# Kernel optimization log

Hardware: AMD Instinct MI355X
Metric: run time of the kernel (lower is better)

The kernel has to match this reference:

```python
import jax, jax.numpy as jnp
import numpy as np

B, IN, C, H, E = 8192, 768, 64, 64, 16  # batch, input_dim, n_concepts, hidden_dim, embedding_dim


def setup_inputs() -> dict:
    key = jax.random.key(0)
    ks = jax.random.split(key, 10)

    def w(k, shape, fan_in):
        return jax.random.normal(k, shape, jnp.float32) / np.float32(np.sqrt(fan_in))

    inp = {"x": jax.random.normal(ks[0], (B, IN), jnp.float32)}
    i = 1
    for pre, din, dout in (("pos", IN, E), ("neg", IN, E), ("cp", 2 * E, 1)):
        inp[pre + "_W1"] = w(ks[i], (C, din, H), din)
        inp[pre + "_b1"] = jnp.zeros((C, H), jnp.float32)
        inp[pre + "_W2"] = w(ks[i + 1], (C, H, H), H)
        inp[pre + "_b2"] = jnp.zeros((C, H), jnp.float32)
        inp[pre + "_W3"] = w(ks[i + 2], (C, H, dout), H)
        inp[pre + "_b3"] = jnp.zeros((C, dout), jnp.float32)
        i += 3
    return inp


def _bank(x, W1, b1, W2, b2, W3, b3):
    # x: [B, IN]; per-concept MLP batched over C via einsum -> [B, C, E]
    h = jax.nn.relu(jnp.einsum('bi,cih->bch', x, W1) + b1)
    h = jax.nn.relu(jnp.einsum('bch,cho->bco', h, W2) + b2)
    return jnp.einsum('bch,che->bce', h, W3) + b3


def reference(x, pos_W1, pos_b1, pos_W2, pos_b2, pos_W3, pos_b3,
              neg_W1, neg_b1, neg_W2, neg_b2, neg_W3, neg_b3,
              cp_W1, cp_b1, cp_W2, cp_b2, cp_W3, cp_b3):
    pos = _bank(x, pos_W1, pos_b1, pos_W2, pos_b2, pos_W3, pos_b3)  # [B,C,E]
    neg = _bank(x, neg_W1, neg_b1, neg_W2, neg_b2, neg_W3, neg_b3)  # [B,C,E]
    # torch cat([pos, neg], dim=1) on [B,E,C], then x[:,:,i] -> per-concept [B, 2E]
    xc = jnp.concatenate([pos, neg], axis=-1)  # [B,C,2E]
    h = jax.nn.relu(jnp.einsum('bci,cih->bch', xc, cp_W1) + cp_b1)
    h = jax.nn.relu(jnp.einsum('bch,cho->bco', h, cp_W2) + cp_b2)
    concepts = (jnp.einsum('bch,cho->bco', h, cp_W3) + cp_b3)[..., 0]  # [B,C]
    w = jnp.clip(concepts * 0.5 + 0.5, 0.0, 1.0)[:, :, None]  # gate in [0,1]
    emb = pos * w + neg * (1.0 - w)  # [B,C,E]
    # torch layout is [B,E,C] then .view(B,-1): transpose before flattening
    emb_flat = jnp.transpose(emb, (0, 2, 1)).reshape(x.shape[0], E * C)
    return emb_flat, concepts
```

## Files before the change

### kernel.cpp

```cpp
#include <hip/hip_runtime.h>
#include <hip/hip_bf16.h>


#define B_   8192
#define IN_  768
#define C_   64
#define H_   64
#define E_   16
#define BM_  128

typedef __bf16 bf16x8 __attribute__((ext_vector_type(8)));
typedef float  f32x4  __attribute__((ext_vector_type(4)));

__device__ __forceinline__ f32x4 mfma16(bf16x8 a, bf16x8 b, f32x4 c) {
  return __builtin_amdgcn_mfma_f32_16x16x32_bf16(a, b, c, 0, 0, 0);
}

__device__ __forceinline__ bf16x8 cvt8(float4 a, float4 b) {
  bf16x8 r;
  r[0] = (__bf16)a.x; r[1] = (__bf16)a.y; r[2] = (__bf16)a.z; r[3] = (__bf16)a.w;
  r[4] = (__bf16)b.x; r[5] = (__bf16)b.y; r[6] = (__bf16)b.z; r[7] = (__bf16)b.w;
  return r;
}

__device__ __forceinline__ void zero_acc(f32x4 (&acc)[2][4]) {
  const f32x4 z = {0.f, 0.f, 0.f, 0.f};
#pragma unroll
  for (int mt = 0; mt < 2; ++mt)
#pragma unroll
    for (int nt = 0; nt < 4; ++nt) acc[mt][nt] = z;
}

__device__ __forceinline__ void gll16(const __bf16* g, __bf16* l) {
  __builtin_amdgcn_global_load_lds(
      (const __attribute__((address_space(1))) unsigned int*)g,
      (__attribute__((address_space(3))) unsigned int*)l, 16, 0, 0);
}

#define FENCE asm volatile("" ::: "memory")

struct __align__(16) SmemT {
  __bf16 bufA[256 * 64];
  __bf16 bufB[256 * 64];
  __bf16 xcb[BM_ * 40];
  float  conc[BM_];
};
static_assert(sizeof(SmemT) == 76288, "layout");
static_assert(sizeof(SmemT) <= 81920, "LDS: need 2 blocks/CU");

__device__ __forceinline__ void epi72(__bf16* __restrict__ hb, f32x4 (&acc)[2][4],
                                      const float* __restrict__ bias,
                                      int wave, int quad, int l16) {
#pragma unroll
  for (int nt = 0; nt < 4; ++nt) {
    const int col = nt * 16 + l16;
    const float bv = bias[col];
#pragma unroll
    for (int mt = 0; mt < 2; ++mt)
#pragma unroll
      for (int r = 0; r < 4; ++r) {
        int row = wave * 32 + mt * 16 + quad * 4 + r;
        hb[row * 72 + col] = (__bf16)fmaxf(acc[mt][nt][r] + bv, 0.f);
      }
  }
}

__device__ __forceinline__ void gemm64(const __bf16* __restrict__ hb,
                                       const __bf16* __restrict__ wt,
                                       f32x4 (&acc)[2][4], int wave, int quad, int l16) {
#pragma unroll
  for (int ks = 0; ks < 2; ++ks) {
    bf16x8 a[2], bb[4];
#pragma unroll
    for (int mt = 0; mt < 2; ++mt)
      a[mt] = *(const bf16x8*)(hb + (wave * 32 + mt * 16 + l16) * 72 + ks * 32 + quad * 8);
#pragma unroll
    for (int nt = 0; nt < 4; ++nt)
      bb[nt] = *(const bf16x8*)(wt + (nt * 16 + l16) * 72 + ks * 32 + quad * 8);
#pragma unroll
    for (int mt = 0; mt < 2; ++mt)
#pragma unroll
      for (int nt = 0; nt < 4; ++nt)
        acc[mt][nt] = mfma16(a[mt], bb[nt], acc[mt][nt]);
  }
}

__device__ __forceinline__ void stage_w64(const __bf16* __restrict__ Wt,
                                          __bf16* __restrict__ wt, int tid) {
#pragma unroll
  for (int it = 0; it < 2; ++it) {
    int q = tid + it * 256;
    int n = q >> 3, i = q & 7;
    *(uint4*)&wt[n * 72 + i * 8] = *(const uint4*)(Wt + n * 64 + i * 8);
  }
}

__device__ __forceinline__ void l3_tile(const __bf16* __restrict__ hb,
                                        const __bf16* __restrict__ wt16,
                                        __bf16* __restrict__ xcb,
                                        const float* __restrict__ b3, int xc_off,
                                        int wave, int quad, int l16) {
  f32x4 acc3[2];
  { const f32x4 z = {0.f, 0.f, 0.f, 0.f}; acc3[0] = z; acc3[1] = z; }
#pragma unroll
  for (int ks = 0; ks < 2; ++ks) {
    bf16x8 bb = *(const bf16x8*)(wt16 + l16 * 72 + ks * 32 + quad * 8);
#pragma unroll
    for (int mt = 0; mt < 2; ++mt) {
      bf16x8 a = *(const bf16x8*)(hb + (wave * 32 + mt * 16 + l16) * 72 + ks * 32 + quad * 8);
      acc3[mt] = mfma16(a, bb, acc3[mt]);
    }
  }
  const float bv = b3[l16];
#pragma unroll
  for (int mt = 0; mt < 2; ++mt)
#pragma unroll
    for (int r = 0; r < 4; ++r) {
      int row = wave * 32 + mt * 16 + quad * 4 + r;
      xcb[row * 40 + xc_off + l16] = (__bf16)(acc3[mt][r] + bv);
    }
}

__device__ __forceinline__ void l1_step(const __bf16* __restrict__ cbuf,
                                        f32x4 (&accP)[2][4], f32x4 (&accN)[2][4],
                                        int wave, int quad, int l16) {
  const int sx = l16 & 7;
#pragma unroll
  for (int ks = 0; ks < 2; ++ks) {
    const int pc = (((ks * 4 + quad) ^ sx)) * 8;
    bf16x8 a[2], bp[4], bn[4];
#pragma unroll
    for (int mt = 0; mt < 2; ++mt)
      a[mt] = *(const bf16x8*)(cbuf + (wave * 32 + mt * 16 + l16) * 64 + pc);
#pragma unroll
    for (int nt = 0; nt < 4; ++nt) {
      bp[nt] = *(const bf16x8*)(cbuf + (128 + nt * 16 + l16) * 64 + pc);
      bn[nt] = *(const bf16x8*)(cbuf + (192 + nt * 16 + l16) * 64 + pc);
    }
#pragma unroll
    for (int mt = 0; mt < 2; ++mt)
#pragma unroll
      for (int nt = 0; nt < 4; ++nt) {
        accP[mt][nt] = mfma16(a[mt], bp[nt], accP[mt][nt]);
        accN[mt][nt] = mfma16(a[mt], bn[nt], accN[mt][nt]);
      }
  }
}

__global__ __launch_bounds__(256, 2) void cb_fused_t(
    const __bf16* __restrict__ x,
    const __bf16* __restrict__ pW1t, const float* __restrict__ pb1,
    const __bf16* __restrict__ pW2t, const float* __restrict__ pb2,
    const __bf16* __restrict__ pW3t, const float* __restrict__ pb3,
    const __bf16* __restrict__ nW1t, const float* __restrict__ nb1,
    const __bf16* __restrict__ nW2t, const float* __restrict__ nb2,
    const __bf16* __restrict__ nW3t, const float* __restrict__ nb3,
    const __bf16* __restrict__ cW1t, const float* __restrict__ cb1,
    const __bf16* __restrict__ cW2t, const float* __restrict__ cb2,
    const __bf16* __restrict__ cw3,  const float* __restrict__ cb3,
    float* __restrict__ out_emb, float* __restrict__ out_con)
{
  __shared__ SmemT sm;
  const int tid  = threadIdx.x;
  const int wave = tid >> 6, lane = tid & 63;
  const int quad = lane >> 4, l16 = lane & 15;
  const int row0 = blockIdx.x * BM_;
  const int c    = blockIdx.y;
  __bf16* hb = sm.bufA;
  __bf16* wt = sm.bufB;

  const __bf16* pg   = pW1t + (size_t)c * 64 * IN_;
  const __bf16* ng   = nW1t + (size_t)c * 64 * IN_;
  const float*  pb1c = pb1 + c * 64;
  const float*  nb1c = nb1 + c * 64;
  const float*  pb2c = pb2 + c * 64;
  const float*  nb2c = nb2 + c * 64;

  f32x4 accP[2][4]; zero_acc(accP);
  f32x4 accN[2][4]; zero_acc(accN);

  const __bf16* xg = x + (size_t)row0 * IN_;
  const int lrow   = lane >> 3;
  const int lchunk = (lane & 7) ^ lrow;
  const __bf16* gsrc = (wave == 0) ? xg
                     : (wave == 1) ? xg + 64 * IN_
                     : (wave == 2) ? pg : ng;
  const __bf16* gl = gsrc + (size_t)lrow * IN_ + lchunk * 8;
  __bf16* const dA = sm.bufA + wave * 64 * 64;
  __bf16* const dB = sm.bufB + wave * 64 * 64;

#pragma unroll
  for (int j = 0; j < 8; ++j)
    gll16(gl + j * 8 * IN_, dA + j * 8 * 64);

  for (int kt = 0; kt < 11; ++kt) {
    {
      const __bf16* gk = gl + (kt + 1) * 64;
      __bf16* nd = (kt & 1) ? dA : dB;
#pragma unroll
      for (int j = 0; j < 8; ++j)
        gll16(gk + j * 8 * IN_, nd + j * 8 * 64);
    }
    asm volatile("s_waitcnt vmcnt(8)" ::: "memory");
    __builtin_amdgcn_s_barrier();
    __builtin_amdgcn_sched_barrier(0);
    FENCE;
    l1_step((kt & 1) ? sm.bufB : sm.bufA, accP, accN, wave, quad, l16);
    FENCE;
    __builtin_amdgcn_s_barrier();
    __builtin_amdgcn_sched_barrier(0);
    FENCE;
  }
  __syncthreads();
  l1_step(sm.bufB, accP, accN, wave, quad, l16);
  __syncthreads();

  epi72(hb, accP, pb1c, wave, quad, l16);
  stage_w64(pW2t + (size_t)c * 64 * 64, wt, tid);
  stage_w64(nW2t + (size_t)c * 64 * 64, wt + 64 * 72, tid);
  __syncthreads();

  f32x4 acc2P[2][4]; zero_acc(acc2P);
  gemm64(hb, wt, acc2P, wave, quad, l16);
  __syncthreads();

  epi72(hb, accN, nb1c, wave, quad, l16);
  {
    int n = tid >> 3, i = tid & 7;
    const __bf16* src = (n < 16)
        ? (pW3t + (size_t)c * 16 * 64 + n * 64 + i * 8)
        : (nW3t + (size_t)c * 16 * 64 + (n - 16) * 64 + i * 8);
    *(uint4*)&wt[n * 72 + i * 8] = *(const uint4*)src;
  }
  __syncthreads();

  f32x4 acc2N[2][4]; zero_acc(acc2N);
  gemm64(hb, wt + 64 * 72, acc2N, wave, quad, l16);
  __syncthreads();

  epi72(hb, acc2P, pb2c, wave, quad, l16);
  __syncthreads();
  l3_tile(hb, wt, sm.xcb, pb3 + c * 16, 0, wave, quad, l16);
  __syncthreads();

  epi72(hb, acc2N, nb2c, wave, quad, l16);
  __syncthreads();
  l3_tile(hb, wt + 16 * 72, sm.xcb, nb3 + c * 16, 16, wave, quad, l16);
  __syncthreads();

  {
    int n = tid >> 2, i = tid & 3;
    *(uint4*)&wt[n * 72 + i * 8] = *(const uint4*)(cW1t + ((size_t)c * 64 + n) * 32 + i * 8);
  }
  __syncthreads();
  f32x4 acc1[2][4]; zero_acc(acc1);
  {
    bf16x8 a[2], bb[4];
#pragma unroll
    for (int mt = 0; mt < 2; ++mt)
      a[mt] = *(const bf16x8*)&sm.xcb[(wave * 32 + mt * 16 + l16) * 40 + quad * 8];
#pragma unroll
    for (int nt = 0; nt < 4; ++nt)
      bb[nt] = *(const bf16x8*)&wt[(nt * 16 + l16) * 72 + quad * 8];
#pragma unroll
    for (int mt = 0; mt < 2; ++mt)
#pragma unroll
      for (int nt = 0; nt < 4; ++nt)
        acc1[mt][nt] = mfma16(a[mt], bb[nt], acc1[mt][nt]);
  }
  __syncthreads();
  epi72(hb, acc1, cb1 + c * 64, wave, quad, l16);
  stage_w64(cW2t + (size_t)c * 64 * 64, wt, tid);
  __syncthreads();

  f32x4 acc2[2][4]; zero_acc(acc2);
  gemm64(hb, wt, acc2, wave, quad, l16);
  __syncthreads();
  epi72(hb, acc2, cb2 + c * 64, wave, quad, l16);
  if (tid < 8) *(uint4*)&wt[tid * 8] = *(const uint4*)(cw3 + (size_t)c * 64 + tid * 8);
  __syncthreads();

  f32x4 acc3[2];
  { const f32x4 z = {0.f, 0.f, 0.f, 0.f}; acc3[0] = z; acc3[1] = z; }
#pragma unroll
  for (int ks = 0; ks < 2; ++ks) {
    bf16x8 bb = {};
    if (l16 == 0) bb = *(const bf16x8*)&wt[ks * 32 + quad * 8];
#pragma unroll
    for (int mt = 0; mt < 2; ++mt) {
      bf16x8 a = *(const bf16x8*)&hb[(wave * 32 + mt * 16 + l16) * 72 + ks * 32 + quad * 8];
      acc3[mt] = mfma16(a, bb, acc3[mt]);
    }
  }
  if (l16 == 0) {
    float bv = cb3[c];
#pragma unroll
    for (int mt = 0; mt < 2; ++mt)
#pragma unroll
      for (int r = 0; r < 4; ++r)
        sm.conc[wave * 32 + mt * 16 + quad * 4 + r] = acc3[mt][r] + bv;
  }
  __syncthreads();

  for (int ii = tid; ii < BM_ * E_; ii += 256) {
    int row = ii >> 4, e = ii & 15;
    float cv = sm.conc[row];
    float w  = fminf(fmaxf(cv * 0.5f + 0.5f, 0.f), 1.f);
    float pv2 = (float)sm.xcb[row * 40 + e];
    float nv2 = (float)sm.xcb[row * 40 + 16 + e];
    out_emb[(size_t)(row0 + row) * (E_ * C_) + e * C_ + c] = pv2 * w + nv2 * (1.f - w);
  }
  if (tid < 128) out_con[(size_t)(row0 + tid) * C_ + c] = sm.conc[tid];
}

#define TSEG 5
#define PSEG 5
struct PrepArgs {
  const float* tsrc[TSEG];
  __bf16*      tdst[TSEG];
  int tstart[TSEG + 1];
  int ktiles[TSEG];
  const float* psrc[PSEG];
  __bf16*      pdst[PSEG];
  int pstart[PSEG + 1];
  int pchunks[PSEG];
  int kdiv8[PSEG];
  int N[PSEG];
  int tblocks;
};

__global__ __launch_bounds__(256) void prep_all(PrepArgs a) {
  const int tid = threadIdx.x;
  const int b = blockIdx.x;
  __shared__ __bf16 lt[64 * 72];
  if (b < a.tblocks) {
    int s = 0;
    while (s < TSEG - 1 && b >= a.tstart[s + 1]) ++s;
    const int idx = b - a.tstart[s];
    const int kt = idx % a.ktiles[s];
    const int c  = idx / a.ktiles[s];
    const int K  = a.ktiles[s] * 64;
    const float* src = a.tsrc[s] + (size_t)c * K * 64 + (size_t)kt * 64 * 64;
    __bf16*      dst = a.tdst[s] + (size_t)c * 64 * K + kt * 64;
    const int r = tid >> 4, c4 = (tid & 15) * 4;
#pragma unroll
    for (int it = 0; it < 4; ++it) {
      int k = r + it * 16;
      float4 v = *(const float4*)(src + (size_t)k * 64 + c4);
      lt[(c4 + 0) * 72 + k] = (__bf16)v.x;
      lt[(c4 + 1) * 72 + k] = (__bf16)v.y;
      lt[(c4 + 2) * 72 + k] = (__bf16)v.z;
      lt[(c4 + 3) * 72 + k] = (__bf16)v.w;
    }
    __syncthreads();
    const int n = tid >> 3, i = tid & 7;
#pragma unroll
    for (int it = 0; it < 2; ++it) {
      int nn = n + it * 32;
      *(uint4*)(dst + (size_t)nn * K + i * 8) = *(const uint4*)&lt[nn * 72 + i * 8];
    }
  } else {
    const int bb = b - a.tblocks;
    int s = 0;
    while (s < PSEG - 1 && bb >= a.pstart[s + 1]) ++s;
    const int lb  = bb - a.pstart[s];
    const int nch = a.pchunks[s];
    const int kc  = a.kdiv8[s];
    const int N   = a.N[s];
#pragma unroll
    for (int j = 0; j < 4; ++j) {
      const int li = (lb * 4 + j) * 256 + tid;
      if (li >= nch) break;
      if (N == 1) {
        const float4* src = (const float4*)a.psrc[s] + (size_t)li * 2;
        float4 v0 = src[0], v1 = src[1];
        *(uint4*)(a.pdst[s] + (size_t)li * 8) = __builtin_bit_cast(uint4, cvt8(v0, v1));
      } else {
        int rn = li / kc;
        int k0 = (li - rn * kc) * 8;
        int cc = rn / N;
        int n  = rn - cc * N;
        const float* src = a.psrc[s] + ((size_t)cc * kc * 8 + k0) * N + n;
        bf16x8 r;
#pragma unroll
        for (int jj = 0; jj < 8; ++jj) r[jj] = (__bf16)src[(size_t)jj * N];
        *(uint4*)(a.pdst[s] + (size_t)rn * kc * 8 + k0) = __builtin_bit_cast(uint4, r);
      }
    }
  }
}

extern "C" void kernel_launch(void* const* d_in, const int* in_sizes, int n_in,
                              void* d_out, int out_size, void* d_ws, size_t ws_size,
                              hipStream_t stream) {
  const float* xf   = (const float*)d_in[0];
  const float* pW1f = (const float*)d_in[1];
  const float* pb1f = (const float*)d_in[2];
  const float* pW2f = (const float*)d_in[3];
  const float* pb2f = (const float*)d_in[4];
  const float* pW3f = (const float*)d_in[5];
  const float* pb3f = (const float*)d_in[6];
  const float* nW1f = (const float*)d_in[7];
  const float* nb1f = (const float*)d_in[8];
  const float* nW2f = (const float*)d_in[9];
  const float* nb2f = (const float*)d_in[10];
  const float* nW3f = (const float*)d_in[11];
  const float* nb3f = (const float*)d_in[12];
  const float* cW1f = (const float*)d_in[13];
  const float* cb1f = (const float*)d_in[14];
  const float* cW2f = (const float*)d_in[15];
  const float* cb2f = (const float*)d_in[16];
  const float* cW3f = (const float*)d_in[17];
  const float* cb3f = (const float*)d_in[18];

  float* out_emb = (float*)d_out;
  float* out_con = out_emb + (size_t)B_ * E_ * C_;

  const int cx   = B_ * IN_;
  const int cW1c = C_ * IN_ * H_;
  const int cW2c = C_ * H_ * H_;
  const int cW3c = C_ * H_ * E_;
  const int ccW1 = C_ * 2 * E_ * H_;
  const int ccW3 = C_ * H_;

  __bf16* w = (__bf16*)d_ws;
  size_t o = 0;
  __bf16* xw   = w + o; o += cx;
  __bf16* pw1t = w + o; o += cW1c;
  __bf16* nw1t = w + o; o += cW1c;
  __bf16* pw2t = w + o; o += cW2c;
  __bf16* nw2t = w + o; o += cW2c;
  __bf16* cw2t = w + o; o += cW2c;
  __bf16* pw3t = w + o; o += cW3c;
  __bf16* nw3t = w + o; o += cW3c;
  __bf16* cw1t = w + o; o += ccW1;
  __bf16* cw3w = w + o; o += ccW3;

  PrepArgs a;
  int tb = 0, pb = 0;
  {
    const float* tsrc[TSEG] = {pW1f, nW1f, pW2f, nW2f, cW2f};
    __bf16*      tdst[TSEG] = {pw1t, nw1t, pw2t, nw2t, cw2t};
    const int    tk[TSEG]   = {12,   12,   1,    1,    1};
    for (int i = 0; i < TSEG; ++i) {
      a.tsrc[i] = tsrc[i]; a.tdst[i] = tdst[i]; a.ktiles[i] = tk[i];
      a.tstart[i] = tb;
      tb += tk[i] * C_;
    }
    a.tstart[TSEG] = tb;
    a.tblocks = tb;

    const float* psrc[PSEG] = {xf, cW3f, pW3f, nW3f, cW1f};
    __bf16*      pdst[PSEG] = {xw, cw3w, pw3t, nw3t, cw1t};
    const int    pKs[PSEG]  = {0,  0,    64,   64,   32};
    const int    pNs[PSEG]  = {1,  1,    16,   16,   64};
    const int    pels[PSEG] = {cx, ccW3, cW3c, cW3c, ccW1};
    for (int i = 0; i < PSEG; ++i) {
      a.psrc[i] = psrc[i]; a.pdst[i] = pdst[i];
      a.pchunks[i] = pels[i] / 8;
      a.kdiv8[i] = (pNs[i] == 1) ? (pels[i] / 8) : (pKs[i] / 8);
      a.N[i] = pNs[i];
      a.pstart[i] = pb;
      pb += (pels[i] / 8 + 1023) / 1024;
    }
    a.pstart[PSEG] = pb;
  }
  prep_all<<<tb + pb, 256, 0, stream>>>(a);

  dim3 grid(B_ / BM_, C_);
  cb_fused_t<<<grid, 256, 0, stream>>>(xw,
      pw1t, pb1f, pw2t, pb2f, pw3t, pb3f,
      nw1t, nb1f, nw2t, nb2f, nw3t, nb3f,
      cw1t, cb1f, cw2t, cb2f, cw3w, cb3f,
      out_emb, out_con);
}
```

Measured before the change: 334.5 us.

## Prefetch tail-layer weights asynchronously and drop per-layer block barriers

While the last layer-1 tile is being computed, each wave issues asynchronous global-to-LDS loads for all remaining per-concept weights (W2, W3, cp W1/W2, cp W3) into a dedicated XOR-swizzled region. The hidden activations now use a 64-wide swizzled layout instead of padded 72-wide rows. Separate pos and neg buffers let the later MLP layers run back to back. Because each wave only touches its own 32 rows, most __syncthreads between layers are removed, cutting the serialized staging and barrier cost in the tail. The risk is that correctness depends on those asynchronous weight loads being complete and visible to all waves before first use, and no explicit full vmcnt wait is visible for them.

```diff
diff --git a/kernel.cpp b/kernel.cpp
--- a/kernel.cpp
+++ b/kernel.cpp
@@ -37,6 +37,16 @@
       (__attribute__((address_space(3))) unsigned int*)l, 16, 0, 0);
 }
 
+__device__ __forceinline__ void gll_w64(const __bf16* M, __bf16* dst, int rbase, int lane) {
+  const int lr = lane >> 3, lc = (lane & 7) ^ lr;
+  gll16(M + (size_t)(rbase + lr) * 64 + lc * 8, dst + rbase * 64);
+}
+
+__device__ __forceinline__ void gll_w32(const __bf16* M, __bf16* dst, int rbase, int lane) {
+  const int lr = lane >> 2, lc = (lane & 3) ^ (lr & 3);
+  gll16(M + (size_t)(rbase + lr) * 32 + lc * 8, dst + rbase * 32);
+}
+
 #define FENCE asm volatile("" ::: "memory")
 
 struct __align__(16) SmemT {
@@ -44,39 +54,43 @@
   __bf16 bufB[256 * 64];
   __bf16 xcb[BM_ * 40];
   float  conc[BM_];
+  __bf16 cw3s[64];
 };
-static_assert(sizeof(SmemT) == 76288, "layout");
+static_assert(sizeof(SmemT) == 76416, "layout");
 static_assert(sizeof(SmemT) <= 81920, "LDS: need 2 blocks/CU");
 
-__device__ __forceinline__ void epi72(__bf16* __restrict__ hb, f32x4 (&acc)[2][4],
-                                      const float* __restrict__ bias,
-                                      int wave, int quad, int l16) {
+__device__ __forceinline__ void epi64s(__bf16* hb, f32x4 (&acc)[2][4],
+                                       const float* __restrict__ bias,
+                                       int wave, int quad, int l16) {
 #pragma unroll
   for (int nt = 0; nt < 4; ++nt) {
-    const int col = nt * 16 + l16;
-    const float bv = bias[col];
+    const int ch = nt * 2 + (l16 >> 3);
+    const int cl = l16 & 7;
+    const float bv = bias[nt * 16 + l16];
 #pragma unroll
     for (int mt = 0; mt < 2; ++mt)
 #pragma unroll
       for (int r = 0; r < 4; ++r) {
-        int row = wave * 32 + mt * 16 + quad * 4 + r;
-        hb[row * 72 + col] = (__bf16)fmaxf(acc[mt][nt][r] + bv, 0.f);
+        const int row = wave * 32 + mt * 16 + quad * 4 + r;
+        hb[row * 64 + (((ch ^ (row & 7)) << 3) | cl)] =
+            (__bf16)fmaxf(acc[mt][nt][r] + bv, 0.f);
       }
   }
 }
 
-__device__ __forceinline__ void gemm64(const __bf16* __restrict__ hb,
-                                       const __bf16* __restrict__ wt,
-                                       f32x4 (&acc)[2][4], int wave, int quad, int l16) {
+__device__ __forceinline__ void gemm64s(const __bf16* A, const __bf16* Bm,
+                                        f32x4 (&acc)[2][4], int wave, int quad, int l16) {
+  const int s7 = l16 & 7;
 #pragma unroll
   for (int ks = 0; ks < 2; ++ks) {
+    const int off = ((ks * 4 + quad) ^ s7) * 8;
     bf16x8 a[2], bb[4];
 #pragma unroll
     for (int mt = 0; mt < 2; ++mt)
-      a[mt] = *(const bf16x8*)(hb + (wave * 32 + mt * 16 + l16) * 72 + ks * 32 + quad * 8);
+      a[mt] = *(const bf16x8*)(A + (wave * 32 + mt * 16 + l16) * 64 + off);
 #pragma unroll
     for (int nt = 0; nt < 4; ++nt)
-      bb[nt] = *(const bf16x8*)(wt + (nt * 16 + l16) * 72 + ks * 32 + quad * 8);
+      bb[nt] = *(const bf16x8*)(Bm + (nt * 16 + l16) * 64 + off);
 #pragma unroll
     for (int mt = 0; mt < 2; ++mt)
 #pragma unroll
@@ -85,29 +99,19 @@
   }
 }
 
-__device__ __forceinline__ void stage_w64(const __bf16* __restrict__ Wt,
-                                          __bf16* __restrict__ wt, int tid) {
-#pragma unroll
-  for (int it = 0; it < 2; ++it) {
-    int q = tid + it * 256;
-    int n = q >> 3, i = q & 7;
-    *(uint4*)&wt[n * 72 + i * 8] = *(const uint4*)(Wt + n * 64 + i * 8);
-  }
-}
-
-__device__ __forceinline__ void l3_tile(const __bf16* __restrict__ hb,
-                                        const __bf16* __restrict__ wt16,
-                                        __bf16* __restrict__ xcb,
-                                        const float* __restrict__ b3, int xc_off,
-                                        int wave, int quad, int l16) {
+__device__ __forceinline__ void l3s(const __bf16* A, const __bf16* B16,
+                                    __bf16* xcb, const float* __restrict__ b3,
+                                    int xc_off, int wave, int quad, int l16) {
+  const int s7 = l16 & 7;
   f32x4 acc3[2];
   { const f32x4 z = {0.f, 0.f, 0.f, 0.f}; acc3[0] = z; acc3[1] = z; }
 #pragma unroll
   for (int ks = 0; ks < 2; ++ks) {
-    bf16x8 bb = *(const bf16x8*)(wt16 + l16 * 72 + ks * 32 + quad * 8);
+    const int off = ((ks * 4 + quad) ^ s7) * 8;
+    bf16x8 bb = *(const bf16x8*)(B16 + l16 * 64 + off);
 #pragma unroll
     for (int mt = 0; mt < 2; ++mt) {
-      bf16x8 a = *(const bf16x8*)(hb + (wave * 32 + mt * 16 + l16) * 72 + ks * 32 + quad * 8);
+      bf16x8 a = *(const bf16x8*)(A + (wave * 32 + mt * 16 + l16) * 64 + off);
       acc3[mt] = mfma16(a, bb, acc3[mt]);
     }
   }
@@ -116,18 +120,18 @@
   for (int mt = 0; mt < 2; ++mt)
 #pragma unroll
     for (int r = 0; r < 4; ++r) {
-      int row = wave * 32 + mt * 16 + quad * 4 + r;
+      const int row = wave * 32 + mt * 16 + quad * 4 + r;
       xcb[row * 40 + xc_off + l16] = (__bf16)(acc3[mt][r] + bv);
     }
 }
 
-__device__ __forceinline__ void l1_step(const __bf16* __restrict__ cbuf,
+__device__ __forceinline__ void l1_step(const __bf16* cbuf,
                                         f32x4 (&accP)[2][4], f32x4 (&accN)[2][4],
                                         int wave, int quad, int l16) {
   const int sx = l16 & 7;
 #pragma unroll
   for (int ks = 0; ks < 2; ++ks) {
-    const int pc = (((ks * 4 + quad) ^ sx)) * 8;
+    const int pc = ((ks * 4 + quad) ^ sx) * 8;
     bf16x8 a[2], bp[4], bn[4];
 #pragma unroll
     for (int mt = 0; mt < 2; ++mt)
@@ -166,8 +170,6 @@
   const int quad = lane >> 4, l16 = lane & 15;
   const int row0 = blockIdx.x * BM_;
   const int c    = blockIdx.y;
-  __bf16* hb = sm.bufA;
-  __bf16* wt = sm.bufB;
 
   const __bf16* pg   = pW1t + (size_t)c * 64 * IN_;
   const __bf16* ng   = nW1t + (size_t)c * 64 * IN_;
@@ -211,48 +213,65 @@
     __builtin_amdgcn_sched_barrier(0);
     FENCE;
   }
+
+  {
+    __bf16* WT = sm.bufA;
+    if (wave == 0) {
+      const __bf16* M = pW2t + (size_t)c * 4096;
+#pragma unroll
+      for (int g = 0; g < 8; ++g) gll_w64(M, WT, g * 8, lane);
+      if (lane < 8) gll16(cw3 + (size_t)c * 64 + lane * 8, sm.cw3s);
+    } else if (wave == 1) {
+      const __bf16* M = nW2t + (size_t)c * 4096;
+#pragma unroll
+      for (int g = 0; g < 8; ++g) gll_w64(M, WT + 4096, g * 8, lane);
+    } else if (wave == 2) {
+      const __bf16* m3p = pW3t + (size_t)c * 1024;
+      const __bf16* m3n = nW3t + (size_t)c * 1024;
+      const __bf16* mc1 = cW1t + (size_t)c * 2048;
+      gll_w64(m3p, WT + 8192, 0, lane);
+      gll_w64(m3p, WT + 8192, 8, lane);
+      gll_w64(m3n, WT + 9216, 0, lane);
+      gll_w64(m3n, WT + 9216, 8, lane);
+      gll_w32(mc1, WT + 10240, 0,  lane);
+      gll_w32(mc1, WT + 10240, 16, lane);
+      gll_w32(mc1, WT + 10240, 32, lane);
+      gll_w32(mc1, WT + 10240, 48, lane);
+    } else {
+      const __bf16* M = cW2t + (size_t)c * 4096;
+#pragma unroll
+      for (int g = 0; g < 8; ++g) gll_w64(M, WT + 12288, g * 8, lane);
+    }
+  }
+
+  asm volatile("s_waitcnt vmcnt(8)" ::: "memory");
+  __builtin_amdgcn_s_barrier();
+  __builtin_amdgcn_sched_barrier(0);
+  FENCE;
+  l1_step(sm.bufB, accP, accN, wave, quad, l16);
+  FENCE;
+  __builtin_amdgcn_s_barrier();
+  __builtin_amdgcn_sched_barrier(0);
+  FENCE;
+
+  __bf16* WT  = sm.bufA;
+  __bf16* hbP = sm.bufB;
+  __bf16* hbN = sm.bufB + 8192;
+
+  epi64s(hbP, accP, pb1c, wave, quad, l16);
+  epi64s(hbN, accN, nb1c, wave, quad, l16);
   __syncthreads();
-  l1_step(sm.bufB, accP, accN, wave, quad, l16);
-  __syncthreads();
-
-  epi72(hb, accP, pb1c, wave, quad, l16);
-  stage_w64(pW2t + (size_t)c * 64 * 64, wt, tid);
-  stage_w64(nW2t + (size_t)c * 64 * 64, wt + 64 * 72, tid);
-  __syncthreads();
 
   f32x4 acc2P[2][4]; zero_acc(acc2P);
-  gemm64(hb, wt, acc2P, wave, quad, l16);
-  __syncthreads();
-
-  epi72(hb, accN, nb1c, wave, quad, l16);
-  {
-    int n = tid >> 3, i = tid & 7;
-    const __bf16* src = (n < 16)
-        ? (pW3t + (size_t)c * 16 * 64 + n * 64 + i * 8)
-        : (nW3t + (size_t)c * 16 * 64 + (n - 16) * 64 + i * 8);
-    *(uint4*)&wt[n * 72 + i * 8] = *(const uint4*)src;
-  }
-  __syncthreads();
-
   f32x4 acc2N[2][4]; zero_acc(acc2N);
-  gemm64(hb, wt + 64 * 72, acc2N, wave, quad, l16);
-  __syncthreads();
-
-  epi72(hb, acc2P, pb2c, wave, quad, l16);
-  __syncthreads();
-  l3_tile(hb, wt, sm.xcb, pb3 + c * 16, 0, wave, quad, l16);
-  __syncthreads();
-
-  epi72(hb, acc2N, nb2c, wave, quad, l16);
-  __syncthreads();
-  l3_tile(hb, wt + 16 * 72, sm.xcb, nb3 + c * 16, 16, wave, quad, l16);
-  __syncthreads();
-
-  {
-    int n = tid >> 2, i = tid & 3;
-    *(uint4*)&wt[n * 72 + i * 8] = *(const uint4*)(cW1t + ((size_t)c * 64 + n) * 32 + i * 8);
-  }
-  __syncthreads();
+  gemm64s(hbP, WT,        acc2P, wave, quad, l16);
+  gemm64s(hbN, WT + 4096, acc2N, wave, quad, l16);
+  epi64s(hbP, acc2P, pb2c, wave, quad, l16);
+  epi64s(hbN, acc2N, nb2c, wave, quad, l16);
+
+  l3s(hbP, WT + 8192, sm.xcb, pb3 + c * 16, 0,  wave, quad, l16);
+  l3s(hbN, WT + 9216, sm.xcb, nb3 + c * 16, 16, wave, quad, l16);
+
   f32x4 acc1[2][4]; zero_acc(acc1);
   {
     bf16x8 a[2], bb[4];
@@ -261,44 +280,43 @@
       a[mt] = *(const bf16x8*)&sm.xcb[(wave * 32 + mt * 16 + l16) * 40 + quad * 8];
 #pragma unroll
     for (int nt = 0; nt < 4; ++nt)
-      bb[nt] = *(const bf16x8*)&wt[(nt * 16 + l16) * 72 + quad * 8];
+      bb[nt] = *(const bf16x8*)(WT + 10240 + (nt * 16 + l16) * 32 +
+                                ((quad ^ (l16 & 3)) * 8));
 #pragma unroll
     for (int mt = 0; mt < 2; ++mt)
 #pragma unroll
       for (int nt = 0; nt < 4; ++nt)
         acc1[mt][nt] = mfma16(a[mt], bb[nt], acc1[mt][nt]);
   }
-  __syncthreads();
-  epi72(hb, acc1, cb1 + c * 64, wave, quad, l16);
-  stage_w64(cW2t + (size_t)c * 64 * 64, wt, tid);
-  __syncthreads();
-
-  f32x4 acc2[2][4]; zero_acc(acc2);
-  gemm64(hb, wt, acc2, wave, quad, l16);
-  __syncthreads();
-  epi72(hb, acc2, cb2 + c * 64, wave, quad, l16);
-  if (tid < 8) *(uint4*)&wt[tid * 8] = *(const uint4*)(cw3 + (size_t)c * 64 + tid * 8);
-  __syncthreads();
-
-  f32x4 acc3[2];
-  { const f32x4 z = {0.f, 0.f, 0.f, 0.f}; acc3[0] = z; acc3[1] = z; }
-#pragma unroll
-  for (int ks = 0; ks < 2; ++ks) {
-    bf16x8 bb = {};
-    if (l16 == 0) bb = *(const bf16x8*)&wt[ks * 32 + quad * 8];
-#pragma unroll
-    for (int mt = 0; mt < 2; ++mt) {
-      bf16x8 a = *(const bf16x8*)&hb[(wave * 32 + mt * 16 + l16) * 72 + ks * 32 + quad * 8];
-      acc3[mt] = mfma16(a, bb, acc3[mt]);
-    }
-  }
-  if (l16 == 0) {
-    float bv = cb3[c];
-#pragma unroll
-    for (int mt = 0; mt < 2; ++mt)
-#pragma unroll
-      for (int r = 0; r < 4; ++r)
-        sm.conc[wave * 32 + mt * 16 + quad * 4 + r] = acc3[mt][r] + bv;
+  epi64s(hbP, acc1, cb1 + c * 64, wave, quad, l16);
+
+  f32x4 accC[2][4]; zero_acc(accC);
+  gemm64s(hbP, WT + 12288, accC, wave, quad, l16);
+  epi64s(hbP, accC, cb2 + c * 64, wave, quad, l16);
+
+  {
+    f32x4 acc3[2];
+    { const f32x4 z = {0.f, 0.f, 0.f, 0.f}; acc3[0] = z; acc3[1] = z; }
+    const int s7 = l16 & 7;
+#pragma unroll
+    for (int ks = 0; ks < 2; ++ks) {
+      const int off = ((ks * 4 + quad) ^ s7) * 8;
+      bf16x8 bb = {};
+      if (l16 == 0) bb = *(const bf16x8*)&sm.cw3s[ks * 32 + quad * 8];
+#pragma unroll
+      for (int mt = 0; mt < 2; ++mt) {
+        bf16x8 a = *(const bf16x8*)(hbP + (wave * 32 + mt * 16 + l16) * 64 + off);
+        acc3[mt] = mfma16(a, bb, acc3[mt]);
+      }
+    }
+    if (l16 == 0) {
+      float bv = cb3[c];
+#pragma unroll
+      for (int mt = 0; mt < 2; ++mt)
+#pragma unroll
+        for (int r = 0; r < 4; ++r)
+          sm.conc[wave * 32 + mt * 16 + quad * 4 + r] = acc3[mt][r] + bv;
+    }
   }
   __syncthreads();
 
```

New measurement: 314.2 us. -6.1%, faster.
